# Kernel tuning notes

Measured on AMD Instinct MI355X. Metric: run time of the kernel, lower is better.

The kernel has to match this reference:

```python
import jax, jax.numpy as jnp
import numpy as np

H = 4
NEG_SLOPE = 0.2
N_P, N_A = 100000, 100000
E = 500000
L = 200000
F_IN, F_HID, F_OUT = 128, 128, 64


def setup_inputs() -> dict:
    key = jax.random.key(0)
    ks = jax.random.split(key, 32)
    s = 0.1  # weight init scale
    inp = {
        'x_paper': jax.random.normal(ks[0], (N_P, F_IN), jnp.float32),
        'x_author': jax.random.normal(ks[1], (N_A, F_IN), jnp.float32),
        'ei_pa': jax.random.randint(ks[2], (2, E), 0, N_P, jnp.int32),
        'ei_ap': jax.random.randint(ks[3], (2, E), 0, N_A, jnp.int32),
        'edge_label_index': jax.random.randint(ks[4], (2, L), 0, N_P, jnp.int32),
        # layer 1 params
        'p1W': s * jax.random.normal(ks[5], (F_IN, F_HID), jnp.float32),
        'p1b': jnp.zeros((F_HID,), jnp.float32),
        'a1W': s * jax.random.normal(ks[6], (F_IN, F_HID), jnp.float32),
        'a1b': jnp.zeros((F_HID,), jnp.float32),
        's1pa': s * jax.random.normal(ks[7], (H, F_HID // H), jnp.float32),
        'd1pa': s * jax.random.normal(ks[8], (H, F_HID // H), jnp.float32),
        's1ap': s * jax.random.normal(ks[9], (H, F_HID // H), jnp.float32),
        'd1ap': s * jax.random.normal(ks[10], (H, F_HID // H), jnp.float32),
        'k1W': s * jax.random.normal(ks[11], (F_HID, F_HID), jnp.float32),
        'k1b': jnp.zeros((F_HID,), jnp.float32),
        'q1': s * jax.random.normal(ks[12], (F_HID,), jnp.float32),
        # layer 2 params
        'p2W': s * jax.random.normal(ks[13], (F_HID, F_OUT), jnp.float32),
        'p2b': jnp.zeros((F_OUT,), jnp.float32),
        'a2W': s * jax.random.normal(ks[14], (F_HID, F_OUT), jnp.float32),
        'a2b': jnp.zeros((F_OUT,), jnp.float32),
        's2pa': s * jax.random.normal(ks[15], (H, F_OUT // H), jnp.float32),
        'd2pa': s * jax.random.normal(ks[16], (H, F_OUT // H), jnp.float32),
        's2ap': s * jax.random.normal(ks[17], (H, F_OUT // H), jnp.float32),
        'd2ap': s * jax.random.normal(ks[18], (H, F_OUT // H), jnp.float32),
        'k2W': s * jax.random.normal(ks[19], (F_OUT, F_OUT), jnp.float32),
        'k2b': jnp.zeros((F_OUT,), jnp.float32),
        'q2': s * jax.random.normal(ks[20], (F_OUT,), jnp.float32),
    }
    return inp


def _edge_attn(h_src, h_dst, src, dst, a_src, a_dst, num_dst):
    # h_*: [N, H, D]; a_*: [H, D]. Per-edge node-level GAT-style attention.
    alpha = (jnp.einsum('nhd,hd->nh', h_src, a_src)[src]
             + jnp.einsum('nhd,hd->nh', h_dst, a_dst)[dst])  # [E, H]
    alpha = jnp.where(alpha >= 0, alpha, NEG_SLOPE * alpha)  # leaky_relu
    amax = jax.ops.segment_max(alpha, dst, num_segments=num_dst)
    amax = jnp.where(jnp.isfinite(amax), amax, 0.0)
    ex = jnp.exp(alpha - amax[dst])
    denom = jax.ops.segment_sum(ex, dst, num_segments=num_dst)
    w = ex / (denom[dst] + 1e-16)
    out = jax.ops.segment_sum(h_src[src] * w[:, :, None], dst, num_segments=num_dst)
    return jax.nn.relu(out).reshape(num_dst, -1)  # [N_dst, H*D]


def _group(xs, q, kW, kb):
    # Semantic-level attention over metapaths (PyG HANConv `group`).
    out = jnp.stack(xs)  # [M, N, F]
    score = (q * jnp.tanh(out @ kW + kb).mean(axis=1)).sum(-1)  # [M]
    attn = jax.nn.softmax(score)
    return (attn[:, None, None] * out).sum(0)


def _han_layer(x_p, x_a, ei_pa, ei_ap, pW, pb, aW, ab, s_pa, d_pa, s_ap, d_ap, kW, kb, q):
    D = pW.shape[1] // H
    h_p = (x_p @ pW + pb).reshape(-1, H, D)
    h_a = (x_a @ aW + ab).reshape(-1, H, D)
    out_a = _edge_attn(h_p, h_a, ei_pa[0], ei_pa[1], s_pa, d_pa, h_a.shape[0])
    out_p = _edge_attn(h_a, h_p, ei_ap[0], ei_ap[1], s_ap, d_ap, h_p.shape[0])
    z_p = _group([out_p], q, kW, kb)
    z_a = _group([out_a], q, kW, kb)
    return z_p, z_a


def reference(x_paper, x_author, ei_pa, ei_ap, edge_label_index,
              p1W, p1b, a1W, a1b, s1pa, d1pa, s1ap, d1ap, k1W, k1b, q1,
              p2W, p2b, a2W, a2b, s2pa, d2pa, s2ap, d2ap, k2W, k2b, q2):
    z_p, z_a = _han_layer(x_paper, x_author, ei_pa, ei_ap,
                          p1W, p1b, a1W, a1b, s1pa, d1pa, s1ap, d1ap, k1W, k1b, q1)
    z_p, z_a = _han_layer(z_p, z_a, ei_pa, ei_ap,
                          p2W, p2b, a2W, a2b, s2pa, d2pa, s2ap, d2ap, k2W, k2b, q2)
    src = z_p[edge_label_index[0]]
    dst = z_a[edge_label_index[1]]
    return (src * dst).sum(axis=-1)  # [L]
```

## Files before the change

kernel.cpp:

```cpp
#include <hip/hip_runtime.h>


#define HEADS 4

typedef _Float16 f16x8 __attribute__((ext_vector_type(8)));
typedef _Float16 f16x4 __attribute__((ext_vector_type(4)));
typedef float    f32x4 __attribute__((ext_vector_type(4)));

__device__ __forceinline__ float leaky02(float a) {
    return a >= 0.f ? a : 0.2f * a;
}

__device__ __forceinline__ void prep_one(const float* W, _Float16* Wf, int M, int o) {
    const int NT = M / 16;
    const int v = o & 7, lane = (o >> 3) & 63, jt = o >> 9;
    const int t = jt / NT, j = jt % NT;
    const int k = t * 32 + (lane >> 4) * 8 + v;
    const int n = j * 16 + (lane & 15);
    Wf[o] = (_Float16)W[k * M + n];
}

__global__ __launch_bounds__(256) void prep_w4(
    const float* __restrict__ W1, _Float16* __restrict__ Wf1,
    const float* __restrict__ W2, _Float16* __restrict__ Wf2,
    const float* __restrict__ W3, _Float16* __restrict__ Wf3,
    const float* __restrict__ W4, _Float16* __restrict__ Wf4) {
    int o = blockIdx.x * 256 + threadIdx.x;
    if (o < 16384)       prep_one(W1, Wf1, 128, o);
    else if (o < 32768)  prep_one(W2, Wf2, 128, o - 16384);
    else if (o < 40960)  prep_one(W3, Wf3, 64, o - 32768);
    else if (o < 49152)  prep_one(W4, Wf4, 64, o - 40960);
}

template<int M, bool AHALF>
__global__ __launch_bounds__(512) void gemm_mfma_dual(
    const void* __restrict__ XA, const _Float16* __restrict__ WfA,
    const float* __restrict__ bA, _Float16* __restrict__ outA,
    const float* __restrict__ svA, const float* __restrict__ dvA,
    float* __restrict__ asA, float* __restrict__ adA,
    const void* __restrict__ XB, const _Float16* __restrict__ WfB,
    const float* __restrict__ bB, _Float16* __restrict__ outB,
    const float* __restrict__ svB, const float* __restrict__ dvB,
    float* __restrict__ asB, float* __restrict__ adB,
    int N, int G) {
    constexpr int NT   = M / 16;
    constexpr int D    = M / HEADS;
    constexpr int SA   = 136;
    constexpr int SE   = M + 4;
    constexpr int WFH  = NT * 4 * 64 * 8;
    constexpr int ROWS = 128;
    __shared__ _Float16 lds_a[ROWS * SA];
    __shared__ _Float16 lds_w[WFH];

    const bool second = blockIdx.x >= (unsigned)G;
    const void* __restrict__ X      = second ? XB : XA;
    const _Float16* __restrict__ Wf = second ? WfB : WfA;
    const float* __restrict__ b     = second ? bB : bA;
    _Float16* __restrict__ out      = second ? outB : outA;
    const float* __restrict__ sv    = second ? svB : svA;
    const float* __restrict__ dv    = second ? dvB : dvA;
    float* __restrict__ asb         = second ? asB : asA;
    float* __restrict__ adb         = second ? adB : adA;
    const int b0 = second ? blockIdx.x - G : blockIdx.x;

    const int wave = threadIdx.x >> 6;
    const int lane = threadIdx.x & 63;
    const int m    = lane & 15;
    const int quad = lane >> 4;

    {
        const int base = threadIdx.x * 8;
        #pragma unroll
        for (int it = 0; it < WFH / 4096; ++it) {
            f16x8 v = *(const f16x8*)(Wf + it * 4096 + base);
            *(f16x8*)(lds_w + it * 4096 + base) = v;
        }
    }

    const int nT = (N + ROWS - 1) / ROWS;
    for (int tb = b0; tb < nT; tb += G) {
        const int row0 = tb * ROWS;

        if (AHALF) {
            #pragma unroll
            for (int it = 0; it < 4; ++it) {
                const int r = it * 32 + (threadIdx.x >> 4);
                const int k = (threadIdx.x & 15) * 8;
                int gr = row0 + r; if (gr >= N) gr = N - 1;
                f16x8 v = *(const f16x8*)((const _Float16*)X + (size_t)gr * 128 + k);
                *(f16x8*)(lds_a + r * SA + k) = v;
            }
        } else {
            #pragma unroll
            for (int it = 0; it < 8; ++it) {
                const int r = it * 16 + (threadIdx.x >> 5);
                const int k = (threadIdx.x & 31) * 4;
                int gr = row0 + r; if (gr >= N) gr = N - 1;
                float4 v = *(const float4*)((const float*)X + (size_t)gr * 128 + k);
                f16x4 h = {(_Float16)v.x, (_Float16)v.y, (_Float16)v.z, (_Float16)v.w};
                *(f16x4*)(lds_a + r * SA + k) = h;
            }
        }
        __syncthreads();

        f32x4 acc[NT];
        #pragma unroll
        for (int j = 0; j < NT; ++j) acc[j] = (f32x4){0.f, 0.f, 0.f, 0.f};

        const int ab = (wave * 16 + m) * SA;
        #pragma unroll
        for (int t = 0; t < 4; ++t) {
            f16x8 a = *(const f16x8*)(lds_a + ab + t * 32 + quad * 8);
            #pragma unroll
            for (int j = 0; j < NT; ++j) {
                f16x8 bf = *(const f16x8*)(lds_w + ((t * NT + j) * 64 + lane) * 8);
                acc[j] = __builtin_amdgcn_mfma_f32_16x16x32_f16(a, bf, acc[j], 0, 0, 0);
            }
        }
        __syncthreads();

        #pragma unroll
        for (int j = 0; j < NT; ++j) {
            const float bias = b[j * 16 + m];
            #pragma unroll
            for (int r = 0; r < 4; ++r)
                lds_a[(wave * 16 + quad * 4 + r) * SE + j * 16 + m] =
                    (_Float16)(acc[j][r] + bias);
        }

        {
            const int r  = lane >> 2;
            const int hh = lane & 3;
            float ps = 0.f, pd = 0.f;
            #pragma unroll
            for (int j = 0; j < D / 4; ++j) {
                f16x4 v4 = *(const f16x4*)(&lds_a[(wave * 16 + r) * SE + hh * D + 4 * j]);
                float4 s4 = *(const float4*)(sv + hh * D + 4 * j);
                float4 d4 = *(const float4*)(dv + hh * D + 4 * j);
                const float v0 = (float)v4[0], v1 = (float)v4[1],
                            v2 = (float)v4[2], v3 = (float)v4[3];
                ps += v0 * s4.x + v1 * s4.y + v2 * s4.z + v3 * s4.w;
                pd += v0 * d4.x + v1 * d4.y + v2 * d4.z + v3 * d4.w;
            }
            const int grow = row0 + wave * 16 + r;
            if (grow < N) {
                asb[(size_t)grow * HEADS + hh] = ps;
                adb[(size_t)grow * HEADS + hh] = pd;
            }
        }

        constexpr int LPR = M / 4;
        constexpr int RPI = 64 / LPR;
        const int lr = lane % LPR;
        const int rq = lane / LPR;
        #pragma unroll
        for (int i = 0; i < 16 / RPI; ++i) {
            const int rr = wave * 16 + i * RPI + rq;
            const int grow = row0 + rr;
            if (grow < N) {
                f16x4 v = *(const f16x4*)(&lds_a[rr * SE + lr * 4]);
                *(f16x4*)(out + (size_t)grow * M + lr * 4) = v;
            }
        }
        __syncthreads();
    }
}

__global__ __launch_bounds__(256) void hist_dual(
    const int* __restrict__ dst_pa, const int* __restrict__ dst_ap,
    int* __restrict__ counts, int N, int E) {
    const int eg = blockIdx.x * 256 + threadIdx.x;
    if (eg >= 2 * E) return;
    const int idx = (eg < E) ? dst_pa[eg] : (N + dst_ap[eg - E]);
    atomicAdd(counts + idx, 1);
}

__global__ __launch_bounds__(256) void scan_blk(
    const int* __restrict__ in, int* __restrict__ out,
    int* __restrict__ bsum, int N) {
    __shared__ int sh[256];
    const int base = blockIdx.x * 1024 + threadIdx.x * 4;
    int v[4]; int s = 0;
    #pragma unroll
    for (int j = 0; j < 4; ++j) { v[j] = (base + j < N) ? in[base + j] : 0; s += v[j]; }
    sh[threadIdx.x] = s;
    __syncthreads();
    for (int off = 1; off < 256; off <<= 1) {
        int t = (threadIdx.x >= off) ? sh[threadIdx.x - off] : 0;
        __syncthreads();
        sh[threadIdx.x] += t;
        __syncthreads();
    }
    int run = sh[threadIdx.x] - s;
    #pragma unroll
    for (int j = 0; j < 4; ++j) {
        if (base + j < N) out[base + j] = run;
        run += v[j];
    }
    if (threadIdx.x == 255) bsum[blockIdx.x] = sh[255];
}

__global__ __launch_bounds__(256) void scan_sums(int* __restrict__ bsum, int nb) {
    __shared__ int sh[256];
    int v = (threadIdx.x < nb) ? bsum[threadIdx.x] : 0;
    sh[threadIdx.x] = v;
    __syncthreads();
    for (int off = 1; off < 256; off <<= 1) {
        int t = (threadIdx.x >= off) ? sh[threadIdx.x - off] : 0;
        __syncthreads();
        sh[threadIdx.x] += t;
        __syncthreads();
    }
    if (threadIdx.x < nb) bsum[threadIdx.x] = sh[threadIdx.x] - v;
}

__global__ __launch_bounds__(256) void scan_add(
    int* __restrict__ out, const int* __restrict__ bsum, int N) {
    const int base = blockIdx.x * 1024 + threadIdx.x * 4;
    const int add = bsum[blockIdx.x];
    #pragma unroll
    for (int j = 0; j < 4; ++j)
        if (base + j < N) out[base + j] += add;
}

__global__ __launch_bounds__(256) void scatter_dual(
    const int* __restrict__ src_pa, const int* __restrict__ dst_pa,
    const int* __restrict__ src_ap, const int* __restrict__ dst_ap,
    const int* __restrict__ offsets, int* __restrict__ cursor,
    int* __restrict__ perm, int N, int E) {
    const int eg = blockIdx.x * 256 + threadIdx.x;
    if (eg >= 2 * E) return;
    int idx, val;
    if (eg < E) { idx = dst_pa[eg];         val = src_pa[eg]; }
    else        { idx = N + dst_ap[eg - E]; val = src_ap[eg - E]; }
    const int pos = offsets[idx] + atomicAdd(cursor + idx, 1);
    perm[pos] = val;
}

__global__ __launch_bounds__(256) void deg_hist(
    const int* __restrict__ cnt, int* __restrict__ bhist, int n) {
    __shared__ int lh[64];
    if (threadIdx.x < 64) lh[threadIdx.x] = 0;
    __syncthreads();
    for (int i = blockIdx.x * 256 + threadIdx.x; i < n; i += gridDim.x * 256) {
        int c = cnt[i]; if (c > 63) c = 63;
        atomicAdd(&lh[c], 1);
    }
    __syncthreads();
    if (threadIdx.x < 64) atomicAdd(&bhist[threadIdx.x], lh[threadIdx.x]);
}

__global__ __launch_bounds__(256) void deg_scatter(
    const int* __restrict__ cnt, int* __restrict__ bcur,
    int* __restrict__ order, int n) {
    __shared__ int lh[64];
    __shared__ int lbase[64];
    if (threadIdx.x < 64) lh[threadIdx.x] = 0;
    __syncthreads();
    const int i = blockIdx.x * 256 + threadIdx.x;
    int c = 0, lpos = 0;
    if (i < n) {
        c = cnt[i]; if (c > 63) c = 63;
        lpos = atomicAdd(&lh[c], 1);
    }
    __syncthreads();
    if (threadIdx.x < 64 && lh[threadIdx.x] > 0)
        lbase[threadIdx.x] = atomicAdd(&bcur[threadIdx.x], lh[threadIdx.x]);
    __syncthreads();
    if (i < n) order[lbase[c] + lpos] = i;
}

template<int F, int D>
__global__ __launch_bounds__(256) void csr_attn_agg_dual(
    const int* __restrict__ order,
    const int* __restrict__ perm, const int* __restrict__ offsets,
    const int* __restrict__ counts,
    const float* __restrict__ asrcP, const float* __restrict__ adstP,
    const _Float16* __restrict__ hP, _Float16* __restrict__ outA,
    const float* __restrict__ asrcA, const float* __restrict__ adstA,
    const _Float16* __restrict__ hA, _Float16* __restrict__ outP,
    int N) {
    constexpr int LPN = F / 8;
    const int gid  = blockIdx.x * 256 + threadIdx.x;
    const int slot = gid / LPN;
    const int lane = gid % LPN;
    if (slot >= 2 * N) return;
    const int node_g = order[slot];
    const bool second = node_g >= N;
    const int node = second ? node_g - N : node_g;
    const float* __restrict__ asrc    = second ? asrcA : asrcP;
    const float* __restrict__ adst    = second ? adstA : adstP;
    const _Float16* __restrict__ hsrc = second ? hA : hP;
    _Float16* __restrict__ out        = second ? outP : outA;

    const int start = offsets[node_g];
    const int cnt   = counts[node_g];
    const int f0 = lane * 8;
    const int h  = f0 / D;
    const float ad = adst[(size_t)node * HEADS + h];

    float den = 0.f;
    float acc[8];
    #pragma unroll
    for (int j = 0; j < 8; ++j) acc[j] = 0.f;
    int i = 0;
    for (; i + 4 <= cnt; i += 4) {
        const int s0 = perm[start + i + 0];
        const int s1 = perm[start + i + 1];
        const int s2 = perm[start + i + 2];
        const int s3 = perm[start + i + 3];
        const float a0 = asrc[(size_t)s0 * HEADS + h];
        const float a1 = asrc[(size_t)s1 * HEADS + h];
        const float a2 = asrc[(size_t)s2 * HEADS + h];
        const float a3 = asrc[(size_t)s3 * HEADS + h];
        f16x8 h0 = *(const f16x8*)(hsrc + (size_t)s0 * F + f0);
        f16x8 h1 = *(const f16x8*)(hsrc + (size_t)s1 * F + f0);
        f16x8 h2 = *(const f16x8*)(hsrc + (size_t)s2 * F + f0);
        f16x8 h3 = *(const f16x8*)(hsrc + (size_t)s3 * F + f0);
        const float e0 = __expf(leaky02(a0 + ad));
        const float e1 = __expf(leaky02(a1 + ad));
        const float e2 = __expf(leaky02(a2 + ad));
        const float e3 = __expf(leaky02(a3 + ad));
        den += (e0 + e1) + (e2 + e3);
        #pragma unroll
        for (int j = 0; j < 8; ++j)
            acc[j] += e0 * (float)h0[j] + e1 * (float)h1[j]
                    + e2 * (float)h2[j] + e3 * (float)h3[j];
    }
    for (; i < cnt; ++i) {
        const int s = perm[start + i];
        const float a = leaky02(asrc[(size_t)s * HEADS + h] + ad);
        const float ex = __expf(a);
        den += ex;
        f16x8 hv = *(const f16x8*)(hsrc + (size_t)s * F + f0);
        #pragma unroll
        for (int j = 0; j < 8; ++j)
            acc[j] += ex * (float)hv[j];
    }
    const float inv = 1.f / (den + 1e-16f);
    f16x8 o;
    #pragma unroll
    for (int j = 0; j < 8; ++j)
        o[j] = (_Float16)fmaxf(acc[j] * inv, 0.f);
    *(f16x8*)(out + (size_t)node * F + f0) = o;
}

__global__ __launch_bounds__(256) void edge_dot(
    const int* __restrict__ eli, const _Float16* __restrict__ zp,
    const _Float16* __restrict__ za, float* __restrict__ out, int L) {
    constexpr int LPE = 8;
    const int gid  = blockIdx.x * blockDim.x + threadIdx.x;
    const int e    = gid / LPE;
    const int lane = gid % LPE;
    if (e >= L) return;
    const int p = eli[e], a = eli[(size_t)L + e];
    f16x8 pv = *(const f16x8*)(zp + (size_t)p * 64 + lane * 8);
    f16x8 av = *(const f16x8*)(za + (size_t)a * 64 + lane * 8);
    float s = 0.f;
    #pragma unroll
    for (int j = 0; j < 8; ++j) s += (float)pv[j] * (float)av[j];
    #pragma unroll
    for (int off = 4; off > 0; off >>= 1) s += __shfl_xor(s, off);
    if (lane == 0) out[e] = s;
}

static inline int cdiv(long long a, long long b) { return (int)((a + b - 1) / b); }

extern "C" void kernel_launch(void* const* d_in, const int* in_sizes, int n_in,
                              void* d_out, int out_size, void* d_ws, size_t ws_size,
                              hipStream_t stream) {
    const float* x_p  = (const float*)d_in[0];
    const float* x_a  = (const float*)d_in[1];
    const int* ei_pa  = (const int*)d_in[2];
    const int* ei_ap  = (const int*)d_in[3];
    const int* eli    = (const int*)d_in[4];
    const float* p1W = (const float*)d_in[5];
    const float* p1b = (const float*)d_in[6];
    const float* a1W = (const float*)d_in[7];
    const float* a1b = (const float*)d_in[8];
    const float* s1pa = (const float*)d_in[9];
    const float* d1pa = (const float*)d_in[10];
    const float* s1ap = (const float*)d_in[11];
    const float* d1ap = (const float*)d_in[12];
    const float* p2W = (const float*)d_in[16];
    const float* p2b = (const float*)d_in[17];
    const float* a2W = (const float*)d_in[18];
    const float* a2b = (const float*)d_in[19];
    const float* s2pa = (const float*)d_in[20];
    const float* d2pa = (const float*)d_in[21];
    const float* s2ap = (const float*)d_in[22];
    const float* d2ap = (const float*)d_in[23];

    const int NP = in_sizes[0] / 128;
    const int E  = in_sizes[2] / 2;
    const int L  = in_sizes[4] / 2;
    const int N  = NP;

    char* ws = (char*)d_ws;
    size_t off = 0;
    auto alloc = [&](size_t bytes) -> char* {
        char* p = ws + off;
        off += (bytes + 255) & ~(size_t)255;
        return p;
    };
    _Float16* h_p1   = (_Float16*)alloc((size_t)N * 128 * 2);
    _Float16* h_a1   = (_Float16*)alloc((size_t)N * 128 * 2);
    _Float16* out_p1 = (_Float16*)alloc((size_t)N * 128 * 2);
    _Float16* out_a1 = (_Float16*)alloc((size_t)N * 128 * 2);
    _Float16* h_p2   = (_Float16*)alloc((size_t)N * 64 * 2);
    _Float16* h_a2   = (_Float16*)alloc((size_t)N * 64 * 2);
    _Float16* out_p2 = (_Float16*)alloc((size_t)N * 64 * 2);
    _Float16* out_a2 = (_Float16*)alloc((size_t)N * 64 * 2);
    float* asrc_pa = (float*)alloc((size_t)N * HEADS * 4);
    float* adst_pa = (float*)alloc((size_t)N * HEADS * 4);
    float* asrc_ap = (float*)alloc((size_t)N * HEADS * 4);
    float* adst_ap = (float*)alloc((size_t)N * HEADS * 4);
    _Float16* Wf1p = (_Float16*)alloc(16384 * 2);
    _Float16* Wf1a = (_Float16*)alloc(16384 * 2);
    _Float16* Wf2p = (_Float16*)alloc(8192 * 2);
    _Float16* Wf2a = (_Float16*)alloc(8192 * 2);
    int* cnt2    = (int*)alloc((size_t)2 * N * 4);
    int* cursor2 = (int*)alloc((size_t)2 * N * 4);
    int* bhist   = (int*)alloc(256);
    int* off2    = (int*)alloc((size_t)2 * N * 4);
    int* perm2   = (int*)alloc((size_t)2 * E * 4);
    int* order2  = (int*)alloc((size_t)2 * N * 4);
    int* bsum    = (int*)alloc(256 * 4);

    const int* src_pa = ei_pa;
    const int* dst_pa = ei_pa + E;
    const int* src_ap = ei_ap;
    const int* dst_ap = ei_ap + E;

    const int N2 = 2 * N;
    const int nbScan = cdiv(N2, 1024);

    prep_w4<<<cdiv(49152, 256), 256, 0, stream>>>(p1W, Wf1p, a1W, Wf1a, p2W, Wf2p, a2W, Wf2a);
    hipMemsetAsync(cnt2, 0, ((size_t)4 * N + 64) * 4, stream);
    hist_dual<<<cdiv((long long)2 * E, 256), 256, 0, stream>>>(dst_pa, dst_ap, cnt2, N, E);
    scan_blk<<<nbScan, 256, 0, stream>>>(cnt2, off2, bsum, N2);
    scan_sums<<<1, 256, 0, stream>>>(bsum, nbScan);
    scan_add<<<nbScan, 256, 0, stream>>>(off2, bsum, N2);
    scatter_dual<<<cdiv((long long)2 * E, 256), 256, 0, stream>>>(
        src_pa, dst_pa, src_ap, dst_ap, off2, cursor2, perm2, N, E);
    deg_hist<<<256, 256, 0, stream>>>(cnt2, bhist, N2);
    scan_sums<<<1, 256, 0, stream>>>(bhist, 64);
    deg_scatter<<<cdiv(N2, 256), 256, 0, stream>>>(cnt2, bhist, order2, N2);

    const int G1 = 256;
    const int G2 = 384;

    gemm_mfma_dual<128, false><<<2 * G1, 512, 0, stream>>>(
        x_p, Wf1p, p1b, h_p1, s1pa, d1ap, asrc_pa, adst_ap,
        x_a, Wf1a, a1b, h_a1, s1ap, d1pa, asrc_ap, adst_pa, N, G1);
    csr_attn_agg_dual<128, 32><<<cdiv((long long)N2 * 16, 256), 256, 0, stream>>>(
        order2, perm2, off2, cnt2,
        asrc_pa, adst_pa, h_p1, out_a1,
        asrc_ap, adst_ap, h_a1, out_p1, N);

    gemm_mfma_dual<64, true><<<2 * G2, 512, 0, stream>>>(
        out_p1, Wf2p, p2b, h_p2, s2pa, d2ap, asrc_pa, adst_ap,
        out_a1, Wf2a, a2b, h_a2, s2ap, d2pa, asrc_ap, adst_pa, N, G2);
    csr_attn_agg_dual<64, 16><<<cdiv((long long)N2 * 8, 256), 256, 0, stream>>>(
        order2, perm2, off2, cnt2,
        asrc_pa, adst_pa, h_p2, out_a2,
        asrc_ap, adst_ap, h_a2, out_p2, N);

    edge_dot<<<cdiv((long long)L * 8, 256), 256, 0, stream>>>(
        eli, out_p2, out_a2, (float*)d_out, L);
}
```

Baseline: 458.3 us.

## Make GEMM waves independent with per-wave tiles and register prefetch

```diff
diff --git a/kernel.cpp b/kernel.cpp
--- a/kernel.cpp
+++ b/kernel.cpp
@@ -33,7 +33,7 @@
 }
 
 template<int M, bool AHALF>
-__global__ __launch_bounds__(512) void gemm_mfma_dual(
+__global__ __launch_bounds__(512, AHALF ? 6 : 4) void gemm_mfma_dual(
     const void* __restrict__ XA, const _Float16* __restrict__ WfA,
     const float* __restrict__ bA, _Float16* __restrict__ outA,
     const float* __restrict__ svA, const float* __restrict__ dvA,
@@ -43,13 +43,12 @@
     const float* __restrict__ svB, const float* __restrict__ dvB,
     float* __restrict__ asB, float* __restrict__ adB,
     int N, int G) {
-    constexpr int NT   = M / 16;
-    constexpr int D    = M / HEADS;
-    constexpr int SA   = 136;
-    constexpr int SE   = M + 4;
-    constexpr int WFH  = NT * 4 * 64 * 8;
-    constexpr int ROWS = 128;
-    __shared__ _Float16 lds_a[ROWS * SA];
+    constexpr int NT  = M / 16;
+    constexpr int D   = M / HEADS;
+    constexpr int SA  = 136;
+    constexpr int WFH = NT * 4 * 64 * 8;
+    constexpr int AWH = 16 * SA;
+    __shared__ _Float16 lds_a[8 * AWH];
     __shared__ _Float16 lds_w[WFH];
 
     const bool second = blockIdx.x >= (unsigned)G;
@@ -76,56 +75,87 @@
             *(f16x8*)(lds_w + it * 4096 + base) = v;
         }
     }
-
-    const int nT = (N + ROWS - 1) / ROWS;
-    for (int tb = b0; tb < nT; tb += G) {
-        const int row0 = tb * ROWS;
-
-        if (AHALF) {
+    __syncthreads();
+
+    _Float16* aw = lds_a + wave * AWH;
+    const int GW = G * 8;
+    const int nT = (N + 15) >> 4;
+    int t = b0 * 8 + wave;
+
+    float4 rs[8];
+    f16x8  rh[4];
+
+    auto issue = [&](int tile) {
+        const int row0 = tile * 16;
+        if constexpr (AHALF) {
             #pragma unroll
             for (int it = 0; it < 4; ++it) {
-                const int r = it * 32 + (threadIdx.x >> 4);
-                const int k = (threadIdx.x & 15) * 8;
+                const int r = it * 4 + (lane >> 4);
+                const int c = lane & 15;
                 int gr = row0 + r; if (gr >= N) gr = N - 1;
-                f16x8 v = *(const f16x8*)((const _Float16*)X + (size_t)gr * 128 + k);
-                *(f16x8*)(lds_a + r * SA + k) = v;
+                rh[it] = *(const f16x8*)((const _Float16*)X + (size_t)gr * 128 + c * 8);
             }
         } else {
             #pragma unroll
             for (int it = 0; it < 8; ++it) {
-                const int r = it * 16 + (threadIdx.x >> 5);
-                const int k = (threadIdx.x & 31) * 4;
+                const int r = it * 2 + (lane >> 5);
+                const int c = lane & 31;
                 int gr = row0 + r; if (gr >= N) gr = N - 1;
-                float4 v = *(const float4*)((const float*)X + (size_t)gr * 128 + k);
-                f16x4 h = {(_Float16)v.x, (_Float16)v.y, (_Float16)v.z, (_Float16)v.w};
-                *(f16x4*)(lds_a + r * SA + k) = h;
-            }
-        }
-        __syncthreads();
+                rs[it] = *(const float4*)((const float*)X + (size_t)gr * 128 + c * 4);
+            }
+        }
+    };
+    auto commit = [&]() {
+        if constexpr (AHALF) {
+            #pragma unroll
+            for (int it = 0; it < 4; ++it) {
+                const int r = it * 4 + (lane >> 4);
+                const int c = lane & 15;
+                *(f16x8*)(aw + r * SA + c * 8) = rh[it];
+            }
+        } else {
+            #pragma unroll
+            for (int it = 0; it < 8; ++it) {
+                const int r = it * 2 + (lane >> 5);
+                const int c = lane & 31;
+                f16x4 h = {(_Float16)rs[it].x, (_Float16)rs[it].y,
+                           (_Float16)rs[it].z, (_Float16)rs[it].w};
+                *(f16x4*)(aw + r * SA + c * 4) = h;
+            }
+        }
+    };
+
+    if (t < nT) issue(t);
+    for (; t < nT; t += GW) {
+        const int row0 = t * 16;
+
+        commit();
+
+        f16x8 afr[4];
+        #pragma unroll
+        for (int tt = 0; tt < 4; ++tt)
+            afr[tt] = *(const f16x8*)(aw + m * SA + tt * 32 + quad * 8);
+
+        if (t + GW < nT) issue(t + GW);
 
         f32x4 acc[NT];
         #pragma unroll
         for (int j = 0; j < NT; ++j) acc[j] = (f32x4){0.f, 0.f, 0.f, 0.f};
-
-        const int ab = (wave * 16 + m) * SA;
-        #pragma unroll
-        for (int t = 0; t < 4; ++t) {
-            f16x8 a = *(const f16x8*)(lds_a + ab + t * 32 + quad * 8);
+        #pragma unroll
+        for (int tt = 0; tt < 4; ++tt) {
             #pragma unroll
             for (int j = 0; j < NT; ++j) {
-                f16x8 bf = *(const f16x8*)(lds_w + ((t * NT + j) * 64 + lane) * 8);
-                acc[j] = __builtin_amdgcn_mfma_f32_16x16x32_f16(a, bf, acc[j], 0, 0, 0);
-            }
-        }
-        __syncthreads();
+                f16x8 bf = *(const f16x8*)(lds_w + ((tt * NT + j) * 64 + lane) * 8);
+                acc[j] = __builtin_amdgcn_mfma_f32_16x16x32_f16(afr[tt], bf, acc[j], 0, 0, 0);
+            }
+        }
 
         #pragma unroll
         for (int j = 0; j < NT; ++j) {
             const float bias = b[j * 16 + m];
             #pragma unroll
             for (int r = 0; r < 4; ++r)
-                lds_a[(wave * 16 + quad * 4 + r) * SE + j * 16 + m] =
-                    (_Float16)(acc[j][r] + bias);
+                aw[(quad * 4 + r) * SA + j * 16 + m] = (_Float16)(acc[j][r] + bias);
         }
 
         {
@@ -134,7 +164,7 @@
             float ps = 0.f, pd = 0.f;
             #pragma unroll
             for (int j = 0; j < D / 4; ++j) {
-                f16x4 v4 = *(const f16x4*)(&lds_a[(wave * 16 + r) * SE + hh * D + 4 * j]);
+                f16x4 v4 = *(const f16x4*)(&aw[r * SA + hh * D + 4 * j]);
                 float4 s4 = *(const float4*)(sv + hh * D + 4 * j);
                 float4 d4 = *(const float4*)(dv + hh * D + 4 * j);
                 const float v0 = (float)v4[0], v1 = (float)v4[1],
@@ -142,7 +172,7 @@
                 ps += v0 * s4.x + v1 * s4.y + v2 * s4.z + v3 * s4.w;
                 pd += v0 * d4.x + v1 * d4.y + v2 * d4.z + v3 * d4.w;
             }
-            const int grow = row0 + wave * 16 + r;
+            const int grow = row0 + r;
             if (grow < N) {
                 asb[(size_t)grow * HEADS + hh] = ps;
                 adb[(size_t)grow * HEADS + hh] = pd;
@@ -155,14 +185,13 @@
         const int rq = lane / LPR;
         #pragma unroll
         for (int i = 0; i < 16 / RPI; ++i) {
-            const int rr = wave * 16 + i * RPI + rq;
+            const int rr = i * RPI + rq;
             const int grow = row0 + rr;
             if (grow < N) {
-                f16x4 v = *(const f16x4*)(&lds_a[rr * SE + lr * 4]);
+                f16x4 v = *(const f16x4*)(&aw[rr * SA + lr * 4]);
                 *(f16x4*)(out + (size_t)grow * M + lr * 4) = v;
             }
         }
-        __syncthreads();
     }
 }
 
```

After: 586.4 us. +27.9%, slower.
